# Optimization experiments

Measured on AMD Instinct MI355X. Metric: run time of the kernel, lower is better.

## Reference

```python
import jax, jax.numpy as jnp
import numpy as np

N_HEADS = 4
DIM_HEAD = 32
SCALE = DIM_HEAD ** -0.5
EPS = 1e-5


def setup_inputs() -> dict:
    key = jax.random.key(0)
    ks = jax.random.split(key, 5)
    b, dim, l, h, w = 8, 128, 32, 32, 32
    hidden = N_HEADS * DIM_HEAD  # 128
    return {
        "x": jax.random.normal(ks[0], (b, dim, l, h, w), dtype=jnp.float32),
        "w_qkv": jax.random.normal(ks[1], (3 * hidden, dim), dtype=jnp.float32) * 0.05,
        "w_out": jax.random.normal(ks[2], (dim, hidden), dtype=jnp.float32) * 0.05,
        "b_out": jax.random.normal(ks[3], (dim,), dtype=jnp.float32) * 0.05,
        "gn_gamma": jnp.ones((dim,), dtype=jnp.float32),
        "gn_beta": jnp.zeros((dim,), dtype=jnp.float32),
    }


def reference(x, w_qkv, w_out, b_out, gn_gamma, gn_beta):
    b, dim, l, h_sp, w_sp = x.shape
    n = l * h_sp * w_sp
    hidden = N_HEADS * DIM_HEAD
    xf = x.reshape(b, dim, n)  # flatten spatial -> tokens
    # 1x1 conv == channel matmul: [3*hidden, dim] x [b, dim, n]
    qkv = jnp.einsum('oc,bcn->bon', w_qkv, xf)
    qkv = qkv.reshape(b, 3, N_HEADS, DIM_HEAD, n)
    q, k, v = qkv[:, 0], qkv[:, 1], qkv[:, 2]  # each [b, H, d, n]
    q = jax.nn.softmax(q, axis=2) * SCALE      # softmax over feature dim d
    k = jax.nn.softmax(k, axis=-1)             # softmax over tokens n
    c = jnp.einsum('bhdn,bhen->bhde', k, v)    # [b, H, d, e] tiny context
    out = jnp.einsum('bhde,bhdn->bhen', c, q)  # [b, H, e, n]
    out = out.reshape(b, hidden, n)
    # to_out 1x1 conv + bias
    y = jnp.einsum('oc,bcn->bon', w_out, out) + b_out[None, :, None]
    # GroupNorm(1, dim): normalize over (C, spatial) per sample
    mean = jnp.mean(y, axis=(1, 2), keepdims=True)
    var = jnp.var(y, axis=(1, 2), keepdims=True)
    y = (y - mean) * jax.lax.rsqrt(var + EPS)
    y = y * gn_gamma[None, :, None] + gn_beta[None, :, None]
    return y.reshape(b, dim, l, h_sp, w_sp)
```

## Files before the change

kernel.cpp:

```cpp
#include <hip/hip_runtime.h>

#define BATCH 8
#define DIMC 128
#define NTOT 32768
#define HEADS 4
#define DHEAD 32
#define SCALE_Q 0.17677669529663687f
#define GRIDX 64
#define TILES 8

typedef _Float16 half8  __attribute__((ext_vector_type(8)));
typedef _Float16 half4v __attribute__((ext_vector_type(4)));
typedef float    f32x4  __attribute__((ext_vector_type(4)));

#define WS_WQKV 0
#define WS_S    98304
#define WS_Z    229376
#define WS_ST   233472
#define WS_NEED 233536


__global__ void k0_prep(const float* __restrict__ wqkv, char* __restrict__ ws) {
    int i = blockIdx.x * 256 + threadIdx.x;
    _Float16* Wb = (_Float16*)(ws + WS_WQKV);
    float* S  = (float*)(ws + WS_S);
    float* Z  = (float*)(ws + WS_Z);
    float* St = (float*)(ws + WS_ST);
    if (i < 49152) Wb[i] = (_Float16)wqkv[i];
    int j = i - 49152;
    if (j >= 0 && j < 32768) S[j] = 0.f;
    int k = j - 32768;
    if (k >= 0 && k < 1024) Z[k] = 0.f;
    int m = k - 1024;
    if (m >= 0 && m < 16) St[m] = 0.f;
}

__global__ __launch_bounds__(256, 2) void k1_kv(const float* __restrict__ x,
                                                const _Float16* __restrict__ Wb,
                                                float* __restrict__ S,
                                                float* __restrict__ Z) {
    __shared__ _Float16 Xb[64][136];
    __shared__ _Float16 KB[128][64];
    __shared__ _Float16 VB[128][64];
    const int t = threadIdx.x;
    const int lane = t & 63, w = t >> 6, g = lane >> 4, l15 = lane & 15;
    const int b = blockIdx.y;

    half8 af[4][4];
#pragma unroll
    for (int mt = 0; mt < 4; ++mt)
#pragma unroll
        for (int kc = 0; kc < 4; ++kc)
            af[mt][kc] = *(const half8*)(Wb + (size_t)(128 + (w * 4 + mt) * 16 + l15) * 128 + kc * 32 + 8 * g);

    f32x4 sacc[2][2];
#pragma unroll
    for (int dm = 0; dm < 2; ++dm)
#pragma unroll
        for (int en = 0; en < 2; ++en) sacc[dm][en] = (f32x4){0.f, 0.f, 0.f, 0.f};
    float zpart = 0.f;

    const int j4 = t & 15, c0 = t >> 4;
    const int sxw = (j4 & 7) << 3;

    float4 xr[8];
#pragma unroll
    for (int cc = 0; cc < 8; ++cc)
        xr[cc] = *(const float4*)(x + ((size_t)b * DIMC + c0 + 16 * cc) * NTOT + blockIdx.x * 64 + 4 * j4);
#pragma unroll
    for (int cc = 0; cc < 8; ++cc) {
        const int c = c0 + 16 * cc;
        Xb[4 * j4 + 0][c ^ sxw] = (_Float16)xr[cc].x;
        Xb[4 * j4 + 1][c ^ sxw] = (_Float16)xr[cc].y;
        Xb[4 * j4 + 2][c ^ sxw] = (_Float16)xr[cc].z;
        Xb[4 * j4 + 3][c ^ sxw] = (_Float16)xr[cc].w;
    }

    for (int it = 0; it < TILES; ++it) {
        if (it < TILES - 1) {
            const int j0n = (blockIdx.x + GRIDX * (it + 1)) * 64;
#pragma unroll
            for (int cc = 0; cc < 8; ++cc)
                xr[cc] = *(const float4*)(x + ((size_t)b * DIMC + c0 + 16 * cc) * NTOT + j0n + 4 * j4);
        }
        __syncthreads();
        half8 bf[4][4];
#pragma unroll
        for (int nt = 0; nt < 4; ++nt) {
            const int sb = ((4 * nt + (l15 >> 2)) & 7) << 3;
#pragma unroll
            for (int kc = 0; kc < 4; ++kc)
                bf[nt][kc] = *(const half8*)(&Xb[nt * 16 + l15][(kc * 32 + 8 * g) ^ sb]);
        }
#pragma unroll
        for (int mt = 0; mt < 4; ++mt) {
            f32x4 a0 = (f32x4){0.f,0.f,0.f,0.f}, a1 = a0, a2 = a0, a3 = a0;
#pragma unroll
            for (int kc = 0; kc < 4; ++kc) {
                a0 = __builtin_amdgcn_mfma_f32_16x16x32_f16(af[mt][kc], bf[0][kc], a0, 0, 0, 0);
                a1 = __builtin_amdgcn_mfma_f32_16x16x32_f16(af[mt][kc], bf[1][kc], a1, 0, 0, 0);
                a2 = __builtin_amdgcn_mfma_f32_16x16x32_f16(af[mt][kc], bf[2][kc], a2, 0, 0, 0);
                a3 = __builtin_amdgcn_mfma_f32_16x16x32_f16(af[mt][kc], bf[3][kc], a3, 0, 0, 0);
            }
            const int lr0 = (w * 4 + mt) * 16 + g * 4;
            const int skv = (((w * 4 + mt) * 4 + g) & 7) << 3;
#pragma unroll
            for (int nt = 0; nt < 4; ++nt) {
                const f32x4 a = (nt == 0) ? a0 : (nt == 1) ? a1 : (nt == 2) ? a2 : a3;
                const int jn = (nt * 16 + l15) ^ skv;
                if (lr0 < 128) {
#pragma unroll
                    for (int r = 0; r < 4; ++r) KB[lr0 + r][jn] = (_Float16)__expf(a[r]);
                } else {
#pragma unroll
                    for (int r = 0; r < 4; ++r) VB[lr0 - 128 + r][jn] = (_Float16)a[r];
                }
            }
        }
        __syncthreads();
        if (it < TILES - 1) {
#pragma unroll
            for (int cc = 0; cc < 8; ++cc) {
                const int c = c0 + 16 * cc;
                Xb[4 * j4 + 0][c ^ sxw] = (_Float16)xr[cc].x;
                Xb[4 * j4 + 1][c ^ sxw] = (_Float16)xr[cc].y;
                Xb[4 * j4 + 2][c ^ sxw] = (_Float16)xr[cc].z;
                Xb[4 * j4 + 3][c ^ sxw] = (_Float16)xr[cc].w;
            }
        }
#pragma unroll
        for (int dm = 0; dm < 2; ++dm) {
            const int sr = ((4 * dm + (l15 >> 2)) & 7) << 3;
#pragma unroll
            for (int en = 0; en < 2; ++en)
#pragma unroll
                for (int kc = 0; kc < 2; ++kc) {
                    half8 ka = *(const half8*)(&KB[w * 32 + dm * 16 + l15][(kc * 32 + 8 * g) ^ sr]);
                    half8 vb = *(const half8*)(&VB[w * 32 + en * 16 + l15][(kc * 32 + 8 * g) ^ sr]);
                    sacc[dm][en] = __builtin_amdgcn_mfma_f32_16x16x32_f16(ka, vb, sacc[dm][en], 0, 0, 0);
                }
        }
        {
            const int zr = lane >> 1;
            const int sz = ((zr >> 2) & 7) << 3;
#pragma unroll
            for (int s8 = 0; s8 < 4; ++s8) {
                half8 hv = *(const half8*)(&KB[w * 32 + zr][((lane & 1) * 32 + 8 * s8) ^ sz]);
#pragma unroll
                for (int e = 0; e < 8; ++e) zpart += (float)hv[e];
            }
        }
    }
    {
        float zt = zpart + __shfl_xor(zpart, 1);
        if ((lane & 1) == 0) atomicAdd(&Z[(b * HEADS + w) * DHEAD + (lane >> 1)], zt);
    }
#pragma unroll
    for (int dm = 0; dm < 2; ++dm)
#pragma unroll
        for (int en = 0; en < 2; ++en)
#pragma unroll
            for (int r = 0; r < 4; ++r)
                atomicAdd(&S[((size_t)(b * HEADS + w) * DHEAD + dm * 16 + g * 4 + r) * DHEAD + en * 16 + l15],
                          sacc[dm][en][r]);
}

__global__ __launch_bounds__(256) void k2_g(const float* __restrict__ S, const float* __restrict__ Z,
                                            const float* __restrict__ wout, char* __restrict__ ybase) {
    __shared__ float Sd[32][33];
    const int h = blockIdx.x, b = blockIdx.y;
    const int t = threadIdx.x;
    const float* Sb = S + (size_t)(b * HEADS + h) * 1024;
    const float* Zb = Z + (size_t)(b * HEADS + h) * 32;
    for (int i = t; i < 1024; i += 256) {
        int d = i >> 5;
        Sd[d][i & 31] = Sb[i] / Zb[d];
    }
    __syncthreads();
    const int o = t & 127, dh = (t >> 7) * 16;
    float wrow[32];
#pragma unroll
    for (int e = 0; e < 32; ++e) wrow[e] = wout[o * 128 + h * 32 + e];
    _Float16* Gb = (_Float16*)(ybase + (size_t)(b >> 1) * 131072 + (size_t)(b & 1) * 32768);
#pragma unroll
    for (int dd = 0; dd < 16; ++dd) {
        const int d = dh + dd;
        float acc = 0.f;
#pragma unroll
        for (int e = 0; e < 32; ++e) acc = fmaf(wrow[e], Sd[d][e], acc);
        Gb[o * 128 + h * 32 + d] = (_Float16)acc;
    }
}

__global__ __launch_bounds__(256, 2) void k3_main(const float* __restrict__ x,
                                                  const _Float16* __restrict__ Wb,
                                                  const float* __restrict__ b_out,
                                                  char* __restrict__ ybase,
                                                  float* __restrict__ St) {
    __shared__ _Float16 Xb[64][136];
    __shared__ _Float16 qT[64][136];
    __shared__ float red[8];
    const int t = threadIdx.x;
    const int lane = t & 63, w = t >> 6, g = lane >> 4, l15 = lane & 15;
    const int b = blockIdx.y;
    const int j4 = t & 15, c0 = t >> 4;
    const int sxw = (j4 & 7) << 3;

    half8 wa[2][4];
    half8 ga[2][4];
    const _Float16* Gb = (const _Float16*)(ybase + (size_t)(b >> 1) * 131072 + (size_t)(b & 1) * 32768);
#pragma unroll
    for (int mi = 0; mi < 2; ++mi)
#pragma unroll
        for (int kc = 0; kc < 4; ++kc) {
            wa[mi][kc] = *(const half8*)(Wb + (size_t)((w * 2 + mi) * 16 + l15) * 128 + kc * 32 + 8 * g);
            ga[mi][kc] = *(const half8*)(Gb + (size_t)((w * 2 + mi) * 16 + l15) * 128 + kc * 32 + 8 * g);
        }

    float ssum = 0.f, ssq = 0.f;

    float4 xr[8];
#pragma unroll
    for (int cc = 0; cc < 8; ++cc)
        xr[cc] = *(const float4*)(x + ((size_t)b * DIMC + c0 + 16 * cc) * NTOT + blockIdx.x * 64 + 4 * j4);
#pragma unroll
    for (int cc = 0; cc < 8; ++cc) {
        const int c = c0 + 16 * cc;
        Xb[4 * j4 + 0][c ^ sxw] = (_Float16)xr[cc].x;
        Xb[4 * j4 + 1][c ^ sxw] = (_Float16)xr[cc].y;
        Xb[4 * j4 + 2][c ^ sxw] = (_Float16)xr[cc].z;
        Xb[4 * j4 + 3][c ^ sxw] = (_Float16)xr[cc].w;
    }
    __syncthreads();

    for (int it = 0; it < TILES; ++it) {
        const int j0 = (blockIdx.x + GRIDX * it) * 64;
        if (it < TILES - 1) {
            const int j0n = (blockIdx.x + GRIDX * (it + 1)) * 64;
#pragma unroll
            for (int cc = 0; cc < 8; ++cc)
                xr[cc] = *(const float4*)(x + ((size_t)b * DIMC + c0 + 16 * cc) * NTOT + j0n + 4 * j4);
        }
        {
            half8 bf[4][4];
#pragma unroll
            for (int nt = 0; nt < 4; ++nt) {
                const int sb = ((4 * nt + (l15 >> 2)) & 7) << 3;
#pragma unroll
                for (int kc = 0; kc < 4; ++kc)
                    bf[nt][kc] = *(const half8*)(&Xb[nt * 16 + l15][(kc * 32 + 8 * g) ^ sb]);
            }
            f32x4 eacc[2][4];
#pragma unroll
            for (int mi = 0; mi < 2; ++mi)
#pragma unroll
                for (int nt = 0; nt < 4; ++nt) eacc[mi][nt] = (f32x4){0.f, 0.f, 0.f, 0.f};
#pragma unroll
            for (int mi = 0; mi < 2; ++mi)
#pragma unroll
                for (int kc = 0; kc < 4; ++kc)
#pragma unroll
                    for (int nt = 0; nt < 4; ++nt)
                        eacc[mi][nt] = __builtin_amdgcn_mfma_f32_16x16x32_f16(wa[mi][kc], bf[nt][kc], eacc[mi][nt], 0, 0, 0);
            float ps[4] = {0.f, 0.f, 0.f, 0.f};
#pragma unroll
            for (int mi = 0; mi < 2; ++mi)
#pragma unroll
                for (int nt = 0; nt < 4; ++nt)
#pragma unroll
                    for (int r = 0; r < 4; ++r) {
                        const float e = __expf(eacc[mi][nt][r]);
                        ps[nt] += e;
                        eacc[mi][nt][r] = e;
                    }
            float scn[4];
#pragma unroll
            for (int nt = 0; nt < 4; ++nt) {
                ps[nt] += __shfl_xor(ps[nt], 16);
                ps[nt] += __shfl_xor(ps[nt], 32);
                scn[nt] = SCALE_Q / ps[nt];
            }
#pragma unroll
            for (int mi = 0; mi < 2; ++mi)
#pragma unroll
                for (int nt = 0; nt < 4; ++nt) {
                    const int sb = ((4 * nt + (l15 >> 2)) & 7) << 3;
                    half4v p;
#pragma unroll
                    for (int r = 0; r < 4; ++r) p[r] = (_Float16)(eacc[mi][nt][r] * scn[nt]);
                    *(half4v*)(&qT[nt * 16 + l15][((w * 2 + mi) * 16 + g * 4) ^ sb]) = p;
                }
        }
        __syncthreads();
        if (it < TILES - 1) {
#pragma unroll
            for (int cc = 0; cc < 8; ++cc) {
                const int c = c0 + 16 * cc;
                Xb[4 * j4 + 0][c ^ sxw] = (_Float16)xr[cc].x;
                Xb[4 * j4 + 1][c ^ sxw] = (_Float16)xr[cc].y;
                Xb[4 * j4 + 2][c ^ sxw] = (_Float16)xr[cc].z;
                Xb[4 * j4 + 3][c ^ sxw] = (_Float16)xr[cc].w;
            }
        }
        {
            half8 bf[4][4];
#pragma unroll
            for (int nt = 0; nt < 4; ++nt) {
                const int sb = ((4 * nt + (l15 >> 2)) & 7) << 3;
#pragma unroll
                for (int kc = 0; kc < 4; ++kc)
                    bf[nt][kc] = *(const half8*)(&qT[nt * 16 + l15][(kc * 32 + 8 * g) ^ sb]);
            }
#pragma unroll
            for (int mi = 0; mi < 2; ++mi) {
                const int o0 = (w * 2 + mi) * 16 + g * 4;
                f32x4 acc[4];
#pragma unroll
                for (int nt = 0; nt < 4; ++nt) acc[nt] = (f32x4){0.f, 0.f, 0.f, 0.f};
#pragma unroll
                for (int kc = 0; kc < 4; ++kc)
#pragma unroll
                    for (int nt = 0; nt < 4; ++nt)
                        acc[nt] = __builtin_amdgcn_mfma_f32_16x16x32_f16(ga[mi][kc], bf[nt][kc], acc[nt], 0, 0, 0);
                float bo[4];
#pragma unroll
                for (int r = 0; r < 4; ++r) bo[r] = b_out[o0 + r];
#pragma unroll
                for (int r = 0; r < 4; ++r) {
                    _Float16* yrow = (_Float16*)(ybase + (size_t)(b * DIMC + o0 + r) * 131072 + 65536);
#pragma unroll
                    for (int nt = 0; nt < 4; ++nt) {
                        const int jn = j0 + nt * 16 + l15;
                        const float yv = acc[nt][r] + bo[r];
                        ssum += yv;
                        ssq += yv * yv;
                        yrow[jn] = (_Float16)yv;
                    }
                }
            }
        }
        __syncthreads();
    }
#pragma unroll
    for (int m = 32; m; m >>= 1) { ssum += __shfl_xor(ssum, m); ssq += __shfl_xor(ssq, m); }
    if (lane == 0) { red[w] = ssum; red[4 + w] = ssq; }
    __syncthreads();
    if (t == 0) {
        atomicAdd(&St[b * 2 + 0], red[0] + red[1] + red[2] + red[3]);
        atomicAdd(&St[b * 2 + 1], red[4] + red[5] + red[6] + red[7]);
    }
}

__global__ __launch_bounds__(256) void k4_norm(float* __restrict__ out, const float* __restrict__ St,
                                               const float* __restrict__ gamma,
                                               const float* __restrict__ beta) {
    const int o = blockIdx.x;
    const int b = blockIdx.y;
    const int t = threadIdx.x;
    const size_t row = (size_t)b * DIMC + o;
    const float n = (float)DIMC * (float)NTOT;
    const float mean = St[b * 2] / n;
    const float var = St[b * 2 + 1] / n - mean * mean;
    const float rs = rsqrtf(var + 1e-5f);
    const float ga = gamma[o] * rs;
    const float be = beta[o];
    const half8* yh = (const half8*)((const char*)out + row * 131072 + 65536);
    half8 hbuf[16];
#pragma unroll
    for (int i = 0; i < 16; ++i) hbuf[i] = yh[i * 256 + t];
    __syncthreads();
    float4* orow = (float4*)(out + row * NTOT);
#pragma unroll
    for (int i = 0; i < 16; ++i) {
        const int e4 = (i * 256 + t) * 2;
        float4 v0, v1;
        v0.x = ((float)hbuf[i][0] - mean) * ga + be;
        v0.y = ((float)hbuf[i][1] - mean) * ga + be;
        v0.z = ((float)hbuf[i][2] - mean) * ga + be;
        v0.w = ((float)hbuf[i][3] - mean) * ga + be;
        v1.x = ((float)hbuf[i][4] - mean) * ga + be;
        v1.y = ((float)hbuf[i][5] - mean) * ga + be;
        v1.z = ((float)hbuf[i][6] - mean) * ga + be;
        v1.w = ((float)hbuf[i][7] - mean) * ga + be;
        orow[e4] = v0;
        orow[e4 + 1] = v1;
    }
}

extern "C" void kernel_launch(void* const* d_in, const int* in_sizes, int n_in,
                              void* d_out, int out_size, void* d_ws, size_t ws_size,
                              hipStream_t stream) {
    const float* x     = (const float*)d_in[0];
    const float* wqkv  = (const float*)d_in[1];
    const float* wout  = (const float*)d_in[2];
    const float* b_out = (const float*)d_in[3];
    const float* gamma = (const float*)d_in[4];
    const float* beta  = (const float*)d_in[5];
    if (ws_size < WS_NEED) return;
    char* ws = (char*)d_ws;
    _Float16* Wb = (_Float16*)(ws + WS_WQKV);
    float* S  = (float*)(ws + WS_S);
    float* Z  = (float*)(ws + WS_Z);
    float* St = (float*)(ws + WS_ST);

    k0_prep<<<325, 256, 0, stream>>>(wqkv, ws);
    k1_kv<<<dim3(GRIDX, 8), 256, 0, stream>>>(x, Wb, S, Z);
    k2_g<<<dim3(HEADS, 8), 256, 0, stream>>>(S, Z, wout, (char*)d_out);
    k3_main<<<dim3(GRIDX, 8), 256, 0, stream>>>(x, Wb, b_out, (char*)d_out, St);
    k4_norm<<<dim3(128, 8), 256, 0, stream>>>((float*)d_out, St, gamma, beta);
}
```

Measured before the change: 138.2 us.

## Compute Q softmax in KV pass, stash fp16 Q, fold G into main kernel

The Q projection and its feature-dim softmax move into the K/V kernel, which already has the x tile in LDS. The scaled fp16 Q goes into the first half of each output row. The main kernel no longer rereads x. It reads the half-size stored Q, and each block computes the w_out·S/Z product in registers, which removes the separate k2 launch. The cost is extra global writes and reads of Q through the output buffer, plus redundant per-block G computation with many scalar global loads of S.

```diff
diff --git a/kernel.cpp b/kernel.cpp
--- a/kernel.cpp
+++ b/kernel.cpp
@@ -38,7 +38,8 @@
 __global__ __launch_bounds__(256, 2) void k1_kv(const float* __restrict__ x,
                                                 const _Float16* __restrict__ Wb,
                                                 float* __restrict__ S,
-                                                float* __restrict__ Z) {
+                                                float* __restrict__ Z,
+                                                char* __restrict__ ybase) {
     __shared__ _Float16 Xb[64][136];
     __shared__ _Float16 KB[128][64];
     __shared__ _Float16 VB[128][64];
@@ -47,11 +48,17 @@
     const int b = blockIdx.y;
 
     half8 af[4][4];
+    half8 wa[2][4];
 #pragma unroll
     for (int mt = 0; mt < 4; ++mt)
 #pragma unroll
         for (int kc = 0; kc < 4; ++kc)
             af[mt][kc] = *(const half8*)(Wb + (size_t)(128 + (w * 4 + mt) * 16 + l15) * 128 + kc * 32 + 8 * g);
+#pragma unroll
+    for (int mi = 0; mi < 2; ++mi)
+#pragma unroll
+        for (int kc = 0; kc < 4; ++kc)
+            wa[mi][kc] = *(const half8*)(Wb + (size_t)((w * 2 + mi) * 16 + l15) * 128 + kc * 32 + 8 * g);
 
     f32x4 sacc[2][2];
 #pragma unroll
@@ -77,6 +84,7 @@
     }
 
     for (int it = 0; it < TILES; ++it) {
+        const int j0 = (blockIdx.x + GRIDX * it) * 64;
         if (it < TILES - 1) {
             const int j0n = (blockIdx.x + GRIDX * (it + 1)) * 64;
 #pragma unroll
@@ -91,6 +99,48 @@
 #pragma unroll
             for (int kc = 0; kc < 4; ++kc)
                 bf[nt][kc] = *(const half8*)(&Xb[nt * 16 + l15][(kc * 32 + 8 * g) ^ sb]);
+        }
+        {
+            f32x4 eacc[2][4];
+#pragma unroll
+            for (int mi = 0; mi < 2; ++mi)
+#pragma unroll
+                for (int nt = 0; nt < 4; ++nt) eacc[mi][nt] = (f32x4){0.f, 0.f, 0.f, 0.f};
+#pragma unroll
+            for (int mi = 0; mi < 2; ++mi)
+#pragma unroll
+                for (int kc = 0; kc < 4; ++kc)
+#pragma unroll
+                    for (int nt = 0; nt < 4; ++nt)
+                        eacc[mi][nt] = __builtin_amdgcn_mfma_f32_16x16x32_f16(wa[mi][kc], bf[nt][kc], eacc[mi][nt], 0, 0, 0);
+            float ps[4] = {0.f, 0.f, 0.f, 0.f};
+#pragma unroll
+            for (int mi = 0; mi < 2; ++mi)
+#pragma unroll
+                for (int nt = 0; nt < 4; ++nt)
+#pragma unroll
+                    for (int r = 0; r < 4; ++r) {
+                        const float e = __expf(eacc[mi][nt][r]);
+                        ps[nt] += e;
+                        eacc[mi][nt][r] = e;
+                    }
+            float scn[4];
+#pragma unroll
+            for (int nt = 0; nt < 4; ++nt) {
+                ps[nt] += __shfl_xor(ps[nt], 16);
+                ps[nt] += __shfl_xor(ps[nt], 32);
+                scn[nt] = SCALE_Q / ps[nt];
+            }
+#pragma unroll
+            for (int mi = 0; mi < 2; ++mi)
+#pragma unroll
+                for (int r = 0; r < 4; ++r) {
+                    const int d = (w * 2 + mi) * 16 + g * 4 + r;
+                    _Float16* erow = (_Float16*)(ybase + (size_t)(b * DIMC + d) * 131072);
+#pragma unroll
+                    for (int nt = 0; nt < 4; ++nt)
+                        erow[j0 + nt * 16 + l15] = (_Float16)(eacc[mi][nt][r] * scn[nt]);
+                }
         }
 #pragma unroll
         for (int mt = 0; mt < 4; ++mt) {
@@ -165,71 +215,58 @@
                           sacc[dm][en][r]);
 }
 
-__global__ __launch_bounds__(256) void k2_g(const float* __restrict__ S, const float* __restrict__ Z,
-                                            const float* __restrict__ wout, char* __restrict__ ybase) {
-    __shared__ float Sd[32][33];
-    const int h = blockIdx.x, b = blockIdx.y;
-    const int t = threadIdx.x;
-    const float* Sb = S + (size_t)(b * HEADS + h) * 1024;
-    const float* Zb = Z + (size_t)(b * HEADS + h) * 32;
-    for (int i = t; i < 1024; i += 256) {
-        int d = i >> 5;
-        Sd[d][i & 31] = Sb[i] / Zb[d];
-    }
-    __syncthreads();
-    const int o = t & 127, dh = (t >> 7) * 16;
-    float wrow[32];
-#pragma unroll
-    for (int e = 0; e < 32; ++e) wrow[e] = wout[o * 128 + h * 32 + e];
-    _Float16* Gb = (_Float16*)(ybase + (size_t)(b >> 1) * 131072 + (size_t)(b & 1) * 32768);
-#pragma unroll
-    for (int dd = 0; dd < 16; ++dd) {
-        const int d = dh + dd;
-        float acc = 0.f;
-#pragma unroll
-        for (int e = 0; e < 32; ++e) acc = fmaf(wrow[e], Sd[d][e], acc);
-        Gb[o * 128 + h * 32 + d] = (_Float16)acc;
-    }
-}
-
-__global__ __launch_bounds__(256, 2) void k3_main(const float* __restrict__ x,
-                                                  const _Float16* __restrict__ Wb,
+__global__ __launch_bounds__(256, 2) void k3_main(const float* __restrict__ S,
+                                                  const float* __restrict__ Z,
+                                                  const float* __restrict__ wout,
                                                   const float* __restrict__ b_out,
                                                   char* __restrict__ ybase,
                                                   float* __restrict__ St) {
-    __shared__ _Float16 Xb[64][136];
-    __shared__ _Float16 qT[64][136];
+    __shared__ _Float16 EB[64][136];
     __shared__ float red[8];
     const int t = threadIdx.x;
     const int lane = t & 63, w = t >> 6, g = lane >> 4, l15 = lane & 15;
     const int b = blockIdx.y;
-    const int j4 = t & 15, c0 = t >> 4;
-    const int sxw = (j4 & 7) << 3;
-
-    half8 wa[2][4];
+
     half8 ga[2][4];
-    const _Float16* Gb = (const _Float16*)(ybase + (size_t)(b >> 1) * 131072 + (size_t)(b & 1) * 32768);
-#pragma unroll
-    for (int mi = 0; mi < 2; ++mi)
+    float bo[2][4];
+#pragma unroll
+    for (int mi = 0; mi < 2; ++mi) {
+        const int o = (w * 2 + mi) * 16 + l15;
+#pragma unroll
+        for (int r = 0; r < 4; ++r) bo[mi][r] = b_out[(w * 2 + mi) * 16 + g * 4 + r];
 #pragma unroll
         for (int kc = 0; kc < 4; ++kc) {
-            wa[mi][kc] = *(const half8*)(Wb + (size_t)((w * 2 + mi) * 16 + l15) * 128 + kc * 32 + 8 * g);
-            ga[mi][kc] = *(const half8*)(Gb + (size_t)((w * 2 + mi) * 16 + l15) * 128 + kc * 32 + 8 * g);
-        }
+            float wrow[32];
+#pragma unroll
+            for (int e = 0; e < 32; ++e) wrow[e] = wout[o * 128 + kc * 32 + e];
+            half8 gv;
+#pragma unroll
+            for (int q = 0; q < 8; ++q) {
+                const int dd = 8 * g + q;
+                const float* srow = S + ((size_t)((b * HEADS + kc) * DHEAD + dd)) * DHEAD;
+                const float rz = 1.0f / Z[(b * HEADS + kc) * DHEAD + dd];
+                float acc = 0.f;
+#pragma unroll
+                for (int e = 0; e < 32; ++e) acc = fmaf(wrow[e], srow[e], acc);
+                gv[q] = (_Float16)(acc * rz);
+            }
+            ga[mi][kc] = gv;
+        }
+    }
 
     float ssum = 0.f, ssq = 0.f;
-
-    float4 xr[8];
-#pragma unroll
-    for (int cc = 0; cc < 8; ++cc)
-        xr[cc] = *(const float4*)(x + ((size_t)b * DIMC + c0 + 16 * cc) * NTOT + blockIdx.x * 64 + 4 * j4);
-#pragma unroll
-    for (int cc = 0; cc < 8; ++cc) {
-        const int c = c0 + 16 * cc;
-        Xb[4 * j4 + 0][c ^ sxw] = (_Float16)xr[cc].x;
-        Xb[4 * j4 + 1][c ^ sxw] = (_Float16)xr[cc].y;
-        Xb[4 * j4 + 2][c ^ sxw] = (_Float16)xr[cc].z;
-        Xb[4 * j4 + 3][c ^ sxw] = (_Float16)xr[cc].w;
+    half8 er[4];
+
+#pragma unroll
+    for (int p = 0; p < 4; ++p) {
+        const int idx = p * 256 + t, d = idx >> 3, jj = (idx & 7) * 8;
+        er[p] = *(const half8*)((const _Float16*)(ybase + (size_t)(b * DIMC + d) * 131072) + blockIdx.x * 64 + jj);
+    }
+#pragma unroll
+    for (int p = 0; p < 4; ++p) {
+        const int idx = p * 256 + t, d = idx >> 3, jj = (idx & 7) * 8;
+#pragma unroll
+        for (int e = 0; e < 8; ++e) EB[jj + e][d ^ ((((jj + e) >> 2) & 7) << 3)] = er[p][e];
     }
     __syncthreads();
 
@@ -238,8 +275,10 @@
         if (it < TILES - 1) {
             const int j0n = (blockIdx.x + GRIDX * (it + 1)) * 64;
 #pragma unroll
-            for (int cc = 0; cc < 8; ++cc)
-                xr[cc] = *(const float4*)(x + ((size_t)b * DIMC + c0 + 16 * cc) * NTOT + j0n + 4 * j4);
+            for (int p = 0; p < 4; ++p) {
+                const int idx = p * 256 + t, d = idx >> 3, jj = (idx & 7) * 8;
+                er[p] = *(const half8*)((const _Float16*)(ybase + (size_t)(b * DIMC + d) * 131072) + j0n + jj);
+            }
         }
         {
             half8 bf[4][4];
@@ -248,68 +287,7 @@
                 const int sb = ((4 * nt + (l15 >> 2)) & 7) << 3;
 #pragma unroll
                 for (int kc = 0; kc < 4; ++kc)
-                    bf[nt][kc] = *(const half8*)(&Xb[nt * 16 + l15][(kc * 32 + 8 * g) ^ sb]);
-            }
-            f32x4 eacc[2][4];
-#pragma unroll
-            for (int mi = 0; mi < 2; ++mi)
-#pragma unroll
-                for (int nt = 0; nt < 4; ++nt) eacc[mi][nt] = (f32x4){0.f, 0.f, 0.f, 0.f};
-#pragma unroll
-            for (int mi = 0; mi < 2; ++mi)
-#pragma unroll
-                for (int kc = 0; kc < 4; ++kc)
-#pragma unroll
-                    for (int nt = 0; nt < 4; ++nt)
-                        eacc[mi][nt] = __builtin_amdgcn_mfma_f32_16x16x32_f16(wa[mi][kc], bf[nt][kc], eacc[mi][nt], 0, 0, 0);
-            float ps[4] = {0.f, 0.f, 0.f, 0.f};
-#pragma unroll
-            for (int mi = 0; mi < 2; ++mi)
-#pragma unroll
-                for (int nt = 0; nt < 4; ++nt)
-#pragma unroll
-                    for (int r = 0; r < 4; ++r) {
-                        const float e = __expf(eacc[mi][nt][r]);
-                        ps[nt] += e;
-                        eacc[mi][nt][r] = e;
-                    }
-            float scn[4];
-#pragma unroll
-            for (int nt = 0; nt < 4; ++nt) {
-                ps[nt] += __shfl_xor(ps[nt], 16);
-                ps[nt] += __shfl_xor(ps[nt], 32);
-                scn[nt] = SCALE_Q / ps[nt];
-            }
-#pragma unroll
-            for (int mi = 0; mi < 2; ++mi)
-#pragma unroll
-                for (int nt = 0; nt < 4; ++nt) {
-                    const int sb = ((4 * nt + (l15 >> 2)) & 7) << 3;
-                    half4v p;
-#pragma unroll
-                    for (int r = 0; r < 4; ++r) p[r] = (_Float16)(eacc[mi][nt][r] * scn[nt]);
-                    *(half4v*)(&qT[nt * 16 + l15][((w * 2 + mi) * 16 + g * 4) ^ sb]) = p;
-                }
-        }
-        __syncthreads();
-        if (it < TILES - 1) {
-#pragma unroll
-            for (int cc = 0; cc < 8; ++cc) {
-                const int c = c0 + 16 * cc;
-                Xb[4 * j4 + 0][c ^ sxw] = (_Float16)xr[cc].x;
-                Xb[4 * j4 + 1][c ^ sxw] = (_Float16)xr[cc].y;
-                Xb[4 * j4 + 2][c ^ sxw] = (_Float16)xr[cc].z;
-                Xb[4 * j4 + 3][c ^ sxw] = (_Float16)xr[cc].w;
-            }
-        }
-        {
-            half8 bf[4][4];
-#pragma unroll
-            for (int nt = 0; nt < 4; ++nt) {
-                const int sb = ((4 * nt + (l15 >> 2)) & 7) << 3;
-#pragma unroll
-                for (int kc = 0; kc < 4; ++kc)
-                    bf[nt][kc] = *(const half8*)(&qT[nt * 16 + l15][(kc * 32 + 8 * g) ^ sb]);
+                    bf[nt][kc] = *(const half8*)(&EB[nt * 16 + l15][(kc * 32 + 8 * g) ^ sb]);
             }
 #pragma unroll
             for (int mi = 0; mi < 2; ++mi) {
@@ -322,21 +300,26 @@
 #pragma unroll
                     for (int nt = 0; nt < 4; ++nt)
                         acc[nt] = __builtin_amdgcn_mfma_f32_16x16x32_f16(ga[mi][kc], bf[nt][kc], acc[nt], 0, 0, 0);
-                float bo[4];
-#pragma unroll
-                for (int r = 0; r < 4; ++r) bo[r] = b_out[o0 + r];
 #pragma unroll
                 for (int r = 0; r < 4; ++r) {
                     _Float16* yrow = (_Float16*)(ybase + (size_t)(b * DIMC + o0 + r) * 131072 + 65536);
 #pragma unroll
                     for (int nt = 0; nt < 4; ++nt) {
-                        const int jn = j0 + nt * 16 + l15;
-                        const float yv = acc[nt][r] + bo[r];
+                        const float yv = acc[nt][r] + bo[mi][r];
                         ssum += yv;
                         ssq += yv * yv;
-                        yrow[jn] = (_Float16)yv;
+                        yrow[j0 + nt * 16 + l15] = (_Float16)yv;
                     }
                 }
+            }
+        }
+        __syncthreads();
+        if (it < TILES - 1) {
+#pragma unroll
+            for (int p = 0; p < 4; ++p) {
+                const int idx = p * 256 + t, d = idx >> 3, jj = (idx & 7) * 8;
+#pragma unroll
+                for (int e = 0; e < 8; ++e) EB[jj + e][d ^ ((((jj + e) >> 2) & 7) << 3)] = er[p][e];
             }
         }
         __syncthreads();
@@ -404,8 +387,7 @@
     float* St = (float*)(ws + WS_ST);
 
     k0_prep<<<325, 256, 0, stream>>>(wqkv, ws);
-    k1_kv<<<dim3(GRIDX, 8), 256, 0, stream>>>(x, Wb, S, Z);
-    k2_g<<<dim3(HEADS, 8), 256, 0, stream>>>(S, Z, wout, (char*)d_out);
-    k3_main<<<dim3(GRIDX, 8), 256, 0, stream>>>(x, Wb, b_out, (char*)d_out, St);
+    k1_kv<<<dim3(GRIDX, 8), 256, 0, stream>>>(x, Wb, S, Z, (char*)d_out);
+    k3_main<<<dim3(GRIDX, 8), 256, 0, stream>>>(S, Z, wout, b_out, (char*)d_out, St);
     k4_norm<<<dim3(128, 8), 256, 0, stream>>>((float*)d_out, St, gamma, beta);
 }
```

Result: slower. 371.5 us (+168.9%).
